# Kernel tuning notes

Measured on AMD Instinct MI355X. Metric: run time of the kernel, lower is better.

## Reference

```python
import jax, jax.numpy as jnp
import numpy as np

N_NODES = 100000
N_EDGES = 3200000
HID = 32
N_LAYERS = 3
MAX_Z = 1000
K = 30
N_GRAPHS = 2000
NPG = N_NODES // N_GRAPHS          # 50 nodes per graph (equal-size graphs)
TLD = HID * N_LAYERS + 1           # total_latent_dim = 97
DENSE = ((K - 2) // 2 + 1 - 5 + 1) * 32  # 352


def _init(key, shape, fan_in):
    return jax.random.normal(key, shape, jnp.float32) / np.sqrt(fan_in)


def setup_inputs():
    key = jax.random.key(0)
    ks = jax.random.split(key, 24)
    z = jax.random.randint(ks[0], (N_NODES,), 0, MAX_Z)
    edge_index = jax.random.randint(ks[1], (2, N_EDGES), 0, N_NODES)
    batch = jnp.repeat(jnp.arange(N_GRAPHS), NPG)  # sorted, equal-size graphs
    inp = {"z": z, "edge_index": edge_index, "batch": batch}
    inp["z_table"] = _init(ks[2], (MAX_Z, HID), HID)
    # GCN stack: (in->h), (h->h), (h->h), (h->1)
    dims = [(HID, HID), (HID, HID), (HID, HID), (HID, 1)]
    for i, (di, do) in enumerate(dims):
        inp[f"W{i}"] = _init(ks[3 + 2 * i], (di, do), di)
        inp[f"b{i}"] = jnp.zeros((do,), jnp.float32)
    inp["conv1_w"] = _init(ks[12], (16, 1, TLD), TLD)
    inp["conv1_b"] = jnp.zeros((16,), jnp.float32)
    inp["conv2_w"] = _init(ks[13], (32, 16, 5), 16 * 5)
    inp["conv2_b"] = jnp.zeros((32,), jnp.float32)
    inp["lin1_w"] = _init(ks[14], (DENSE, 128), DENSE)
    inp["lin1_b"] = jnp.zeros((128,), jnp.float32)
    inp["lin2_w"] = _init(ks[15], (128, 1), 128)
    inp["lin2_b"] = jnp.zeros((1,), jnp.float32)
    return inp


def gcn_conv(x, src, dst, W, b):
    # PyG GCNConv: h = x @ W, then symmetric-normalized propagation with self-loops, + bias.
    h = x @ W
    deg = jnp.zeros((N_NODES,), h.dtype).at[dst].add(1.0) + 1.0  # +1 self loop
    dinv = jax.lax.rsqrt(deg)
    coef = dinv[src] * dinv[dst]                                  # [E]
    out = jnp.zeros_like(h).at[dst].add(h[src] * coef[:, None])   # neighbor agg
    out = out + h * (dinv * dinv)[:, None]                        # self-loop term
    return out + b


def conv1d(x, w, b, stride):
    y = jax.lax.conv_general_dilated(x, w, (stride,), 'VALID',
                                     dimension_numbers=('NCH', 'OIH', 'NCH'))
    return y + b[None, :, None]


def sort_pool(x, k):
    # global_sort_pool with equal-size graphs: sort nodes within each graph by
    # last feature channel (descending), keep top-k, flatten.
    xb = x.reshape(N_GRAPHS, NPG, -1)
    order = jnp.argsort(-xb[:, :, -1], axis=1)[:, :k]             # [B, k]
    xk = jnp.take_along_axis(xb, order[:, :, None], axis=1)       # [B, k, D]
    return xk.reshape(N_GRAPHS, -1)


def reference(z, edge_index, batch, z_table, W0, b0, W1, b1, W2, b2, W3, b3,
              conv1_w, conv1_b, conv2_w, conv2_b, lin1_w, lin1_b, lin2_w, lin2_b):
    src, dst = edge_index[0], edge_index[1]
    h = z_table[z]                                   # [N, HID]
    xs = []
    for W, b in ((W0, b0), (W1, b1), (W2, b2), (W3, b3)):
        h = jnp.tanh(gcn_conv(h, src, dst, W, b))
        xs.append(h)
    x = jnp.concatenate(xs, axis=-1)                 # [N, 97]
    x = sort_pool(x, K)[:, None, :]                  # [B, 1, K*97]
    x = jax.nn.relu(conv1d(x, conv1_w, conv1_b, TLD))  # [B, 16, K]
    B, C, L = x.shape
    x = x.reshape(B, C, L // 2, 2).max(-1)           # maxpool1d(2,2) -> [B,16,15]
    x = jax.nn.relu(conv1d(x, conv2_w, conv2_b, 1))  # [B, 32, 11]
    x = x.reshape(B, -1)                             # [B, 352]
    x = jax.nn.relu(x @ lin1_w + lin1_b)             # dropout is identity at eval
    return x @ lin2_w + lin2_b                       # [B, 1]
```

## Files before the change

### kernel.cpp

```cpp
#include <hip/hip_runtime.h>
#include <hip/hip_bf16.h>
#include <math.h>

#define N_NODES 100000
#define N_EDGES 3200000
#define HID 32
#define K_TOP 30
#define N_GRAPHS 2000
#define NPG 50
#define TLD 97
#define DENSE 352

#define NB 256
#define NPB 391
#define CAP 14336
#define CE  ((N_EDGES + 2047) / 2048)

__global__ __launch_bounds__(256) void k_bucket(const int* __restrict__ dst,
                                                const int* __restrict__ src,
                                                int* __restrict__ gcount,
                                                int2* __restrict__ buf) {
    __shared__ int hist[NB];
    __shared__ int base_l[NB];
    int tid = threadIdx.x;
    int e0 = blockIdx.x * CE;
    int e1 = e0 + CE; if (e1 > N_EDGES) e1 = N_EDGES;
    hist[tid] = 0;
    __syncthreads();
    for (int e = e0 + tid; e < e1; e += 256) {
        int d = dst[e];
        atomicAdd(&hist[d / NPB], 1);
    }
    __syncthreads();
    int cnt = hist[tid];
    base_l[tid] = cnt ? atomicAdd(&gcount[tid], cnt) : 0;
    __syncthreads();
    hist[tid] = 0;
    __syncthreads();
    for (int e = e0 + tid; e < e1; e += 256) {
        int d = dst[e];
        int s = src[e];
        int b = d / NPB;
        int r = atomicAdd(&hist[b], 1);
        buf[b * CAP + base_l[b] + r] = int2{d, s};
    }
}

__global__ void k_scan256(const int* __restrict__ gcount, int* __restrict__ bucket_base,
                          int* __restrict__ row_ptr) {
    __shared__ int s[NB];
    int tid = threadIdx.x;
    int v = gcount[tid];
    s[tid] = v;
    __syncthreads();
    for (int off = 1; off < NB; off <<= 1) {
        int t = (tid >= off) ? s[tid - off] : 0;
        __syncthreads();
        s[tid] += t;
        __syncthreads();
    }
    bucket_base[tid] = s[tid] - v;
    if (tid == NB - 1) row_ptr[N_NODES] = s[tid];
}

__global__ __launch_bounds__(512) void k_build(const int2* __restrict__ buf,
                                               const int* __restrict__ gcount,
                                               const int* __restrict__ bucket_base,
                                               int* __restrict__ row_ptr,
                                               float* __restrict__ dinv,
                                               int* __restrict__ col) {
    __shared__ int s[512];
    int k = blockIdx.x;
    int tid = threadIdx.x;
    int lo = k * NPB;
    int cnt = gcount[k];
    int rowbase = bucket_base[k];
    const int2* b = buf + k * CAP;
    s[tid] = 0;
    __syncthreads();
    for (int i = tid; i < cnt; i += 512)
        atomicAdd(&s[b[i].x - lo], 1);
    __syncthreads();
    int mydeg = s[tid];
    bool valid = (tid < NPB) && (lo + tid < N_NODES);
    if (valid) dinv[lo + tid] = rsqrtf((float)(mydeg + 1));
    for (int off = 1; off < 512; off <<= 1) {
        int t = (tid >= off) ? s[tid - off] : 0;
        __syncthreads();
        s[tid] += t;
        __syncthreads();
    }
    int excl = s[tid] - mydeg;
    if (valid) row_ptr[lo + tid] = rowbase + excl;
    __syncthreads();
    s[tid] = excl;
    __syncthreads();
    for (int i = tid; i < cnt; i += 512) {
        int2 e = b[i];
        int r = atomicAdd(&s[e.x - lo], 1);
        col[rowbase + r] = e.y;
    }
}

__global__ void k_embed_lin0(const int* __restrict__ z, const float* __restrict__ zt,
                             const float* __restrict__ W, const float* __restrict__ dinv,
                             float* __restrict__ hs) {
    __shared__ float Ws[32 * 32];
    int tid = threadIdx.x;
    for (int i = tid; i < 1024; i += 256) Ws[i] = W[i];
    __syncthreads();
    int gi = blockIdx.x * 256 + tid;
    if (gi >= N_NODES * 32) return;
    int n = gi >> 5, f = gi & 31;
    float v = zt[z[n] * 32 + f];
    float acc = 0.f;
#pragma unroll
    for (int f2 = 0; f2 < 32; ++f2)
        acc += __shfl(v, f2, 32) * Ws[f2 * 32 + f];
    hs[gi] = acc * dinv[n];
}

__device__ __forceinline__ float gather32(const float* __restrict__ hs,
                                          const int* __restrict__ col,
                                          int beg, int end, int f, float acc) {
    for (int base = beg; base < end; base += 32) {
        int rem = end - base;
        int m = rem >= 32 ? 32 : rem;
        int c = (f < m) ? col[base + f] : 0;
        float vals[32];
#pragma unroll
        for (int i = 0; i < 32; ++i) {
            int ci = __shfl(c, i, 32);
            vals[i] = hs[ci * 32 + f];
        }
        if (m == 32) {
#pragma unroll
            for (int i = 0; i < 32; ++i) acc += vals[i];
        } else {
#pragma unroll
            for (int i = 0; i < 32; ++i)
                if (i < m) acc += vals[i];
        }
    }
    return acc;
}

__global__ void k_layer(const float* __restrict__ hs, const int* __restrict__ row_ptr,
                        const int* __restrict__ col, const float* __restrict__ dinv,
                        const float* __restrict__ b, const float* __restrict__ Wnext,
                        float* __restrict__ xcat, int coloff,
                        float* __restrict__ hs_out) {
    __shared__ float Ws[32 * 32];
    int tid = threadIdx.x;
    for (int i = tid; i < 1024; i += 256) Ws[i] = Wnext[i];
    __syncthreads();
    int gi = blockIdx.x * 256 + tid;
    if (gi >= N_NODES * 32) return;
    int n = gi >> 5, f = gi & 31;
    int beg = row_ptr[n], end = row_ptr[n + 1];
    float acc = hs[n * 32 + f];
    acc = gather32(hs, col, beg, end, f, acc);
    float v = tanhf(acc * dinv[n] + b[f]);
    xcat[n * 97 + coloff + f] = v;
    float a2 = 0.f;
#pragma unroll
    for (int f2 = 0; f2 < 32; ++f2)
        a2 += __shfl(v, f2, 32) * Ws[f2 * 32 + f];
    hs_out[n * 32 + f] = a2 * dinv[n];
}

__global__ void k_layer_last(const float* __restrict__ hs, const int* __restrict__ row_ptr,
                             const int* __restrict__ col, const float* __restrict__ dinv,
                             const float* __restrict__ b, const float* __restrict__ W3,
                             float* __restrict__ xcat, int coloff,
                             float* __restrict__ h4) {
    int gi = blockIdx.x * 256 + threadIdx.x;
    if (gi >= N_NODES * 32) return;
    int n = gi >> 5, f = gi & 31;
    int beg = row_ptr[n], end = row_ptr[n + 1];
    float acc = hs[n * 32 + f];
    acc = gather32(hs, col, beg, end, f, acc);
    float v = tanhf(acc * dinv[n] + b[f]);
    xcat[n * 97 + coloff + f] = v;
    float p = v * W3[f];
#pragma unroll
    for (int off = 16; off >= 1; off >>= 1) p += __shfl_xor(p, off);
    if (f == 0) h4[n] = p * dinv[n];
}

__global__ void k_prop1w(const float* __restrict__ hs4, const int* __restrict__ row_ptr,
                         const int* __restrict__ col, const float* __restrict__ dinv,
                         const float* __restrict__ b3, float* __restrict__ xcat) {
    int gi = blockIdx.x * 256 + threadIdx.x;
    if (gi >= N_NODES * 32) return;
    int n = gi >> 5, lane = gi & 31;
    int beg = row_ptr[n], end = row_ptr[n + 1];
    float part = 0.f;
    for (int e = beg + lane; e < end; e += 32)
        part += hs4[col[e]];
#pragma unroll
    for (int off = 16; off >= 1; off >>= 1) part += __shfl_xor(part, off);
    if (lane == 0) {
        float acc = hs4[n] + part;
        xcat[n * 97 + 96] = tanhf(acc * dinv[n] + b3[0]);
    }
}

__global__ __launch_bounds__(128) void k_head(
    const float* __restrict__ xcat,
    const float* __restrict__ w1, const float* __restrict__ b1,
    const float* __restrict__ w2, const float* __restrict__ b2,
    const float* __restrict__ l1w, const float* __restrict__ l1b,
    const float* __restrict__ l2w, const float* __restrict__ l2b,
    float* __restrict__ out) {
    __shared__ float xk[K_TOP][97];
    __shared__ float w1s[16 * 97];
    __shared__ float w2s[32 * 80];
    __shared__ float y1[16][K_TOP];
    __shared__ float y1p[16][15];
    __shared__ float y2[DENSE];
    __shared__ float z1[128];
    __shared__ int   sel[K_TOP];
    __shared__ float red[2];

    int g = blockIdx.x;
    int tid = threadIdx.x;
    int base = g * NPG;

    for (int i = tid; i < 16 * 97; i += 128) w1s[i] = w1[i];
    for (int i = tid; i < 32 * 80; i += 128) w2s[i] = w2[i];

    if (tid < 64) {
        float v; int idx;
        if (tid < NPG) { v = xcat[(base + tid) * 97 + 96]; idx = tid; }
        else           { v = -INFINITY;                    idx = 64 + tid; }
        for (int k = 2; k <= 64; k <<= 1) {
            for (int j = k >> 1; j > 0; j >>= 1) {
                float ov = __shfl_xor(v, j);
                int   oi = __shfl_xor(idx, j);
                bool lower = (tid & j) == 0;
                bool dirA  = (tid & k) == 0;
                bool mineFirst = (v > ov) || (v == ov && idx < oi);
                bool keep = lower ? (mineFirst == dirA) : (mineFirst != dirA);
                if (!keep) { v = ov; idx = oi; }
            }
        }
        if (tid < K_TOP) sel[tid] = idx;
    }
    __syncthreads();

    for (int i = tid; i < K_TOP * 97; i += 128) {
        int j = i / 97, d = i - j * 97;
        xk[j][d] = xcat[(base + sel[j]) * 97 + d];
    }
    __syncthreads();

    for (int i = tid; i < 16 * K_TOP; i += 128) {
        int c = i / K_TOP, j = i - c * K_TOP;
        float acc = b1[c];
#pragma unroll
        for (int d = 0; d < 97; ++d) acc += xk[j][d] * w1s[c * 97 + d];
        y1[c][j] = fmaxf(acc, 0.f);
    }
    __syncthreads();

    for (int i = tid; i < 16 * 15; i += 128) {
        int c = i / 15, p = i - c * 15;
        y1p[c][p] = fmaxf(y1[c][2 * p], y1[c][2 * p + 1]);
    }
    __syncthreads();

    for (int i = tid; i < 32 * 11; i += 128) {
        int o = i / 11, p = i - o * 11;
        float acc = b2[o];
#pragma unroll
        for (int ci = 0; ci < 16; ++ci)
#pragma unroll
            for (int t = 0; t < 5; ++t)
                acc += y1p[ci][p + t] * w2s[o * 80 + ci * 5 + t];
        y2[o * 11 + p] = fmaxf(acc, 0.f);
    }
    __syncthreads();

    {
        float acc = l1b[tid];
        for (int r = 0; r < DENSE; ++r) acc += y2[r] * l1w[r * 128 + tid];
        z1[tid] = fmaxf(acc, 0.f);
    }
    __syncthreads();

    float p = z1[tid] * l2w[tid];
    for (int off = 32; off >= 1; off >>= 1) p += __shfl_xor(p, off);
    if ((tid & 63) == 0) red[tid >> 6] = p;
    __syncthreads();
    if (tid == 0) out[g] = red[0] + red[1] + l2b[0];
}

extern "C" void kernel_launch(void* const* d_in, const int* in_sizes, int n_in,
                              void* d_out, int out_size, void* d_ws, size_t ws_size,
                              hipStream_t stream) {
    const int*   z   = (const int*)d_in[0];
    const int*   ei  = (const int*)d_in[1];
    const float* zt  = (const float*)d_in[3];
    const float* W0  = (const float*)d_in[4];  const float* b0  = (const float*)d_in[5];
    const float* W1  = (const float*)d_in[6];  const float* b1g = (const float*)d_in[7];
    const float* W2  = (const float*)d_in[8];  const float* b2g = (const float*)d_in[9];
    const float* W3  = (const float*)d_in[10]; const float* b3  = (const float*)d_in[11];
    const float* c1w = (const float*)d_in[12]; const float* c1b = (const float*)d_in[13];
    const float* c2w = (const float*)d_in[14]; const float* c2b = (const float*)d_in[15];
    const float* l1w = (const float*)d_in[16]; const float* l1b = (const float*)d_in[17];
    const float* l2w = (const float*)d_in[18]; const float* l2b = (const float*)d_in[19];
    float* out = (float*)d_out;

    char* ws = (char*)d_ws;
    size_t off = 0;
    auto alloc = [&](size_t bytes) {
        void* p = ws + off;
        off += (bytes + 255) & ~(size_t)255;
        return p;
    };
    int*   row_ptr     = (int*)alloc((size_t)(N_NODES + 1) * 4);
    float* dinv        = (float*)alloc((size_t)N_NODES * 4);
    int*   col         = (int*)alloc((size_t)N_EDGES * 4);
    int*   gcount      = (int*)alloc((size_t)NB * 4);
    int*   bucket_base = (int*)alloc((size_t)NB * 4);
    int2*  bucketbuf   = (int2*)alloc((size_t)NB * CAP * 8);
    float* hA          = (float*)alloc((size_t)N_NODES * 32 * 4);
    float* hB          = (float*)alloc((size_t)N_NODES * 32 * 4);
    float* h4          = (float*)alloc((size_t)N_NODES * 4);
    float* xcat        = (float*)alloc((size_t)N_NODES * 97 * 4);

    const int* srcp = ei;
    const int* dstp = ei + N_EDGES;

    hipMemsetAsync(gcount, 0, (size_t)NB * 4, stream);

    int nf = (N_NODES * 32 + 255) / 256;

    k_bucket<<<2048, 256, 0, stream>>>(dstp, srcp, gcount, bucketbuf);
    k_scan256<<<1, NB, 0, stream>>>(gcount, bucket_base, row_ptr);
    k_build<<<NB, 512, 0, stream>>>(bucketbuf, gcount, bucket_base, row_ptr, dinv, col);

    k_embed_lin0<<<nf, 256, 0, stream>>>(z, zt, W0, dinv, hA);
    k_layer<<<nf, 256, 0, stream>>>(hA, row_ptr, col, dinv, b0, W1, xcat, 0, hB);
    k_layer<<<nf, 256, 0, stream>>>(hB, row_ptr, col, dinv, b1g, W2, xcat, 32, hA);
    k_layer_last<<<nf, 256, 0, stream>>>(hA, row_ptr, col, dinv, b2g, W3, xcat, 64, h4);
    k_prop1w<<<nf, 256, 0, stream>>>(h4, row_ptr, col, dinv, b3, xcat);

    k_head<<<N_GRAPHS, 128, 0, stream>>>(xcat, c1w, c1b, c2w, c2b,
                                         l1w, l1b, l2w, l2b, out);
}
```

Baseline: 490.5 us.

## Pack bucket entries into one int, fold scan into build, fewer bucket blocks

Bucket entries now store the local destination index and the source node together in one 32-bit int (local dst shifted left by 17 bits, src in the low 17 bits), halving the bytes written and read in the bucket buffer. The separate single-block scan kernel is removed: every build block recomputes the 256-entry prefix sum over bucket counts, which saves a launch but repeats a little work per block. The bucket kernel also runs on 512 blocks instead of 2048, so each block covers more edges and fewer global atomics are issued on the bucket counters.

After: 455.8 us. 1.08x faster.

```diff
diff --git a/kernel.cpp b/kernel.cpp
--- a/kernel.cpp
+++ b/kernel.cpp
@@ -14,12 +14,13 @@
 #define NB 256
 #define NPB 391
 #define CAP 14336
-#define CE  ((N_EDGES + 2047) / 2048)
+#define NBLK 512
+#define CE  ((N_EDGES + NBLK - 1) / NBLK)
 
 __global__ __launch_bounds__(256) void k_bucket(const int* __restrict__ dst,
                                                 const int* __restrict__ src,
                                                 int* __restrict__ gcount,
-                                                int2* __restrict__ buf) {
+                                                int* __restrict__ buf) {
     __shared__ int hist[NB];
     __shared__ int base_l[NB];
     int tid = threadIdx.x;
@@ -42,44 +43,36 @@
         int s = src[e];
         int b = d / NPB;
         int r = atomicAdd(&hist[b], 1);
-        buf[b * CAP + base_l[b] + r] = int2{d, s};
-    }
-}
-
-__global__ void k_scan256(const int* __restrict__ gcount, int* __restrict__ bucket_base,
-                          int* __restrict__ row_ptr) {
-    __shared__ int s[NB];
-    int tid = threadIdx.x;
-    int v = gcount[tid];
-    s[tid] = v;
-    __syncthreads();
-    for (int off = 1; off < NB; off <<= 1) {
-        int t = (tid >= off) ? s[tid - off] : 0;
-        __syncthreads();
-        s[tid] += t;
-        __syncthreads();
-    }
-    bucket_base[tid] = s[tid] - v;
-    if (tid == NB - 1) row_ptr[N_NODES] = s[tid];
-}
-
-__global__ __launch_bounds__(512) void k_build(const int2* __restrict__ buf,
+        buf[b * CAP + base_l[b] + r] = ((d - b * NPB) << 17) | s;
+    }
+}
+
+__global__ __launch_bounds__(512) void k_build(const int* __restrict__ buf,
                                                const int* __restrict__ gcount,
-                                               const int* __restrict__ bucket_base,
                                                int* __restrict__ row_ptr,
                                                float* __restrict__ dinv,
                                                int* __restrict__ col) {
+    __shared__ int sb[NB];
     __shared__ int s[512];
     int k = blockIdx.x;
     int tid = threadIdx.x;
+    if (tid < NB) sb[tid] = gcount[tid];
+    __syncthreads();
+    for (int off = 1; off < NB; off <<= 1) {
+        int t = (tid < NB && tid >= off) ? sb[tid - off] : 0;
+        __syncthreads();
+        if (tid < NB) sb[tid] += t;
+        __syncthreads();
+    }
+    int rowbase = (k == 0) ? 0 : sb[k - 1];
+    int cnt = gcount[k];
+    if (k == NB - 1 && tid == 0) row_ptr[N_NODES] = sb[NB - 1];
     int lo = k * NPB;
-    int cnt = gcount[k];
-    int rowbase = bucket_base[k];
-    const int2* b = buf + k * CAP;
+    const int* b = buf + k * CAP;
     s[tid] = 0;
     __syncthreads();
     for (int i = tid; i < cnt; i += 512)
-        atomicAdd(&s[b[i].x - lo], 1);
+        atomicAdd(&s[b[i] >> 17], 1);
     __syncthreads();
     int mydeg = s[tid];
     bool valid = (tid < NPB) && (lo + tid < N_NODES);
@@ -96,9 +89,9 @@
     s[tid] = excl;
     __syncthreads();
     for (int i = tid; i < cnt; i += 512) {
-        int2 e = b[i];
-        int r = atomicAdd(&s[e.x - lo], 1);
-        col[rowbase + r] = e.y;
+        int v = b[i];
+        int r = atomicAdd(&s[v >> 17], 1);
+        col[rowbase + r] = v & 0x1FFFF;
     }
 }
 
@@ -319,16 +312,15 @@
         off += (bytes + 255) & ~(size_t)255;
         return p;
     };
-    int*   row_ptr     = (int*)alloc((size_t)(N_NODES + 1) * 4);
-    float* dinv        = (float*)alloc((size_t)N_NODES * 4);
-    int*   col         = (int*)alloc((size_t)N_EDGES * 4);
-    int*   gcount      = (int*)alloc((size_t)NB * 4);
-    int*   bucket_base = (int*)alloc((size_t)NB * 4);
-    int2*  bucketbuf   = (int2*)alloc((size_t)NB * CAP * 8);
-    float* hA          = (float*)alloc((size_t)N_NODES * 32 * 4);
-    float* hB          = (float*)alloc((size_t)N_NODES * 32 * 4);
-    float* h4          = (float*)alloc((size_t)N_NODES * 4);
-    float* xcat        = (float*)alloc((size_t)N_NODES * 97 * 4);
+    int*   row_ptr   = (int*)alloc((size_t)(N_NODES + 1) * 4);
+    float* dinv      = (float*)alloc((size_t)N_NODES * 4);
+    int*   col       = (int*)alloc((size_t)N_EDGES * 4);
+    int*   gcount    = (int*)alloc((size_t)NB * 4);
+    int*   bucketbuf = (int*)alloc((size_t)NB * CAP * 4);
+    float* hA        = (float*)alloc((size_t)N_NODES * 32 * 4);
+    float* hB        = (float*)alloc((size_t)N_NODES * 32 * 4);
+    float* h4        = (float*)alloc((size_t)N_NODES * 4);
+    float* xcat      = (float*)alloc((size_t)N_NODES * 97 * 4);
 
     const int* srcp = ei;
     const int* dstp = ei + N_EDGES;
@@ -337,9 +329,8 @@
 
     int nf = (N_NODES * 32 + 255) / 256;
 
-    k_bucket<<<2048, 256, 0, stream>>>(dstp, srcp, gcount, bucketbuf);
-    k_scan256<<<1, NB, 0, stream>>>(gcount, bucket_base, row_ptr);
-    k_build<<<NB, 512, 0, stream>>>(bucketbuf, gcount, bucket_base, row_ptr, dinv, col);
+    k_bucket<<<NBLK, 256, 0, stream>>>(dstp, srcp, gcount, bucketbuf);
+    k_build<<<NB, 512, 0, stream>>>(bucketbuf, gcount, row_ptr, dinv, col);
 
     k_embed_lin0<<<nf, 256, 0, stream>>>(z, zt, W0, dinv, hA);
     k_layer<<<nf, 256, 0, stream>>>(hA, row_ptr, col, dinv, b0, W1, xcat, 0, hB);
```
